# Kernel optimization log

Measured on AMD Instinct MI355X. Metric: run time of the kernel, lower is better.

The kernel has to match this reference:

```python
import jax, jax.numpy as jnp
import numpy as np

DEPTH = 2          # number of transformer blocks
DIM = 1280         # hidden_size
NHEADS = 16
HDIM = DIM // NHEADS  # 80
FF = 5120          # intermediate_size
S = 8192           # total ragged tokens
NSEG = 8           # number of image segments
EPS = 1e-6
GRID = 32          # per-image patch grid side (32*32*8 = 8192)


def _rotate_half(x):
    h = x.shape[-1] // 2
    return jnp.concatenate([-x[..., h:], x[..., :h]], axis=-1)


def _layernorm(x, g, b):
    mu = jnp.mean(x, axis=-1, keepdims=True)
    var = jnp.mean(jnp.square(x - mu), axis=-1, keepdims=True)
    return (x - mu) * jax.lax.rsqrt(var + EPS) * g + b


def setup_inputs() -> dict:
    key = jax.random.key(0)
    ks = jax.random.split(key, 16)
    std = 0.02
    hidden_states = jax.random.normal(ks[0], (S, DIM), jnp.float32)
    cu_seqlens = jnp.arange(NSEG + 1, dtype=jnp.int32) * (S // NSEG)
    # 2D rotary: per-axis freq table of size head_dim//4, concat row+col -> head_dim//2,
    # duplicated (cat(freqs, freqs)) -> head_dim, then cos/sin.
    rot_dim = HDIM // 2
    inv_freq = 1.0 / (10000.0 ** (jnp.arange(0, rot_dim, 2, dtype=jnp.float32) / rot_dim))  # [HDIM//4]
    tok = jnp.arange(S)
    rows = ((tok % (GRID * GRID)) // GRID).astype(jnp.float32)
    cols = (tok % GRID).astype(jnp.float32)
    freqs = jnp.concatenate([rows[:, None] * inv_freq[None, :], cols[:, None] * inv_freq[None, :]], axis=-1)  # [S, HDIM//2]
    emb = jnp.concatenate([freqs, freqs], axis=-1)  # [S, HDIM]
    cos = jnp.cos(emb)
    sin = jnp.sin(emb)
    def rnd(k, shape):
        return jax.random.normal(k, shape, jnp.float32) * std
    params = {
        'ln1_g': jnp.ones((DEPTH, DIM), jnp.float32), 'ln1_b': jnp.zeros((DEPTH, DIM), jnp.float32),
        'ln2_g': jnp.ones((DEPTH, DIM), jnp.float32), 'ln2_b': jnp.zeros((DEPTH, DIM), jnp.float32),
        'qkv_w': rnd(ks[1], (DEPTH, 3 * DIM, DIM)), 'qkv_b': jnp.zeros((DEPTH, 3 * DIM), jnp.float32),
        'proj_w': rnd(ks[2], (DEPTH, DIM, DIM)), 'proj_b': jnp.zeros((DEPTH, DIM), jnp.float32),
        'fc1_w': rnd(ks[3], (DEPTH, FF, DIM)), 'fc1_b': jnp.zeros((DEPTH, FF), jnp.float32),
        'fc2_w': rnd(ks[4], (DEPTH, DIM, FF)), 'fc2_b': jnp.zeros((DEPTH, DIM), jnp.float32),
    }
    return dict(hidden_states=hidden_states, cu_seqlens=cu_seqlens, cos=cos, sin=sin, **params)


def reference(hidden_states, cu_seqlens, cos, sin,
              ln1_g, ln1_b, ln2_g, ln2_b,
              qkv_w, qkv_b, proj_w, proj_b,
              fc1_w, fc1_b, fc2_w, fc2_b):
    seq = hidden_states.shape[0]
    # cu_seqlens is a static (int) input; derive the block-diagonal segmentation.
    seg = np.diff(np.asarray(jax.device_get(cu_seqlens)))
    L = int(seg[0])
    assert (seg == L).all(), 'reference assumes equal-length segments'
    n = len(seg)
    scale = HDIM ** -0.5
    c = cos[:, None, :]  # broadcast over heads, like cos.unsqueeze(1)
    s_ = sin[:, None, :]
    x = hidden_states
    for i in range(DEPTH):
        # --- attention ---
        h = _layernorm(x, ln1_g[i], ln1_b[i])
        qkv = (h @ qkv_w[i].T + qkv_b[i]).reshape(seq, 3, NHEADS, HDIM)
        q, k, v = qkv[:, 0], qkv[:, 1], qkv[:, 2]
        q = q * c + _rotate_half(q) * s_
        k = k * c + _rotate_half(k) * s_
        qs = q.reshape(n, L, NHEADS, HDIM)
        ks_ = k.reshape(n, L, NHEADS, HDIM)
        vs = v.reshape(n, L, NHEADS, HDIM)
        # block-diagonal (per-segment) attention, fp32 softmax
        attn = jnp.einsum('nlhd,nkhd->nhlk', qs, ks_) * scale
        p = jax.nn.softmax(attn, axis=-1)
        o = jnp.einsum('nhlk,nkhd->nlhd', p, vs).reshape(seq, DIM)
        x = x + (o @ proj_w[i].T + proj_b[i])
        # --- mlp (gelu tanh approx) ---
        h2 = _layernorm(x, ln2_g[i], ln2_b[i])
        x = x + (jax.nn.gelu(h2 @ fc1_w[i].T + fc1_b[i], approximate=True) @ fc2_w[i].T + fc2_b[i])
    return x
```

## Files before the change

### kernel.cpp

```cpp
#include <hip/hip_runtime.h>
#include <hip/hip_bf16.h>

typedef __attribute__((ext_vector_type(8))) short bf16x8;
typedef __attribute__((ext_vector_type(4))) float f32x4;
typedef __attribute__((ext_vector_type(8))) unsigned short u16x8;

__device__ __forceinline__ void gload_lds16(const void* g, void* l) {
  __builtin_amdgcn_global_load_lds(
      (const __attribute__((address_space(1))) unsigned int*)g,
      (__attribute__((address_space(3))) unsigned int*)l, 16, 0, 0);
}

__device__ __forceinline__ unsigned short f2bfu(float f) {
  __hip_bfloat16 h = __float2bfloat16(f);
  return __builtin_bit_cast(unsigned short, h);
}

__global__ __launch_bounds__(256) void copy_f32(const float* __restrict__ in,
                                                float* __restrict__ out, int n) {
  for (int i = blockIdx.x * 256 + threadIdx.x; i < n; i += gridDim.x * 256)
    out[i] = in[i];
}

__global__ __launch_bounds__(256) void w2bf(const float* __restrict__ in,
                                            __hip_bfloat16* __restrict__ out, int n) {
  for (int i = blockIdx.x * 256 + threadIdx.x; i < n; i += gridDim.x * 256)
    out[i] = __float2bfloat16(in[i]);
}

__global__ __launch_bounds__(256) void ln_kernel(const float* __restrict__ x,
                                                 const float* __restrict__ g,
                                                 const float* __restrict__ b,
                                                 __hip_bfloat16* __restrict__ h) {
  const int row = blockIdx.x;
  const int tid = threadIdx.x;
  const float* xr = x + (size_t)row * 1280;
  float v[5];
  float s = 0.f;
#pragma unroll
  for (int i = 0; i < 5; i++) { v[i] = xr[tid + i * 256]; s += v[i]; }
#pragma unroll
  for (int off = 32; off >= 1; off >>= 1) s += __shfl_xor(s, off);
  __shared__ float red[8];
  const int w = tid >> 6, lane = tid & 63;
  if (lane == 0) red[w] = s;
  __syncthreads();
  const float mu = (red[0] + red[1] + red[2] + red[3]) * (1.f / 1280.f);
  float q = 0.f;
#pragma unroll
  for (int i = 0; i < 5; i++) { float d = v[i] - mu; q += d * d; }
#pragma unroll
  for (int off = 32; off >= 1; off >>= 1) q += __shfl_xor(q, off);
  if (lane == 0) red[4 + w] = q;
  __syncthreads();
  const float var = (red[4] + red[5] + red[6] + red[7]) * (1.f / 1280.f);
  const float rstd = rsqrtf(var + 1e-6f);
#pragma unroll
  for (int i = 0; i < 5; i++) {
    int c = tid + i * 256;
    h[(size_t)row * 1280 + c] = __float2bfloat16((v[i] - mu) * rstd * g[c] + b[c]);
  }
}

__global__ __launch_bounds__(256) void rope_kernel(__hip_bfloat16* __restrict__ qkv,
                                                   const float* __restrict__ cs,
                                                   const float* __restrict__ sn) {
  const int TOT = 8192 * 2 * 16 * 40;
  for (int idx = blockIdx.x * 256 + threadIdx.x; idx < TOT; idx += gridDim.x * 256) {
    int d = idx % 40;
    int t = idx / 40;
    int head = t & 15;
    int t2 = t >> 4;
    int part = t2 & 1;
    int s = t2 >> 1;
    size_t base = ((size_t)s * 3 + part) * 1280 + head * 80;
    float e0 = __bfloat162float(qkv[base + d]);
    float e1 = __bfloat162float(qkv[base + d + 40]);
    float c0 = cs[s * 80 + d];
    float s0 = sn[s * 80 + d];
    float c1 = cs[s * 80 + d + 40];
    float s1 = sn[s * 80 + d + 40];
    qkv[base + d]      = __float2bfloat16(e0 * c0 - e1 * s0);
    qkv[base + d + 40] = __float2bfloat16(e1 * c1 + e0 * s1);
  }
}

__global__ __launch_bounds__(256) void vtrans_kernel(const __hip_bfloat16* __restrict__ qkv,
                                                     __hip_bfloat16* __restrict__ vt) {
  const int idx = blockIdx.x * 256 + threadIdx.x;
  const int s = idx & 8191;
  const int dc = idx >> 13;
  const unsigned short* src = (const unsigned short*)qkv + ((size_t)s * 3 + 2) * 1280 + dc * 8;
  u16x8 v = *(const u16x8*)src;
  unsigned short* dst = (unsigned short*)vt + (size_t)dc * 8 * 8192 + s;
#pragma unroll
  for (int j = 0; j < 8; j++) dst[(size_t)j * 8192] = v[j];
}

#define VMCNT4 asm volatile("s_waitcnt vmcnt(4)" ::: "memory")

#define GPHASE(MH, NH, DOA, STG, VM)                                                       \
  do {                                                                                     \
    if (DOA) {                                                                             \
      _Pragma("unroll") for (int mm = 0; mm < 4; mm++)                                     \
      _Pragma("unroll") for (int kk = 0; kk < 2; kk++)                                     \
        af[mm][kk] = *(const bf16x8*)(lds + bufOff + (MH) * 16384 + rowA + mm * 2048 + sw_s[kk]); \
    }                                                                                      \
    bf16x8 bfr[2][2];                                                                      \
    _Pragma("unroll") for (int nn = 0; nn < 2; nn++)                                       \
    _Pragma("unroll") for (int kk = 0; kk < 2; kk++)                                       \
      bfr[nn][kk] = *(const bf16x8*)(lds + bufOff + (NH) * 16384 + rowB + nn * 2048 + sw_s[kk]); \
    STG;                                                                                   \
    __builtin_amdgcn_s_barrier();                                                          \
    __builtin_amdgcn_s_setprio(1);                                                         \
    _Pragma("unroll") for (int kk = 0; kk < 2; kk++)                                       \
    _Pragma("unroll") for (int mm = 0; mm < 4; mm++)                                       \
    _Pragma("unroll") for (int nn = 0; nn < 2; nn++)                                       \
      acc[(MH) * 4 + mm][(NH) * 2 + nn] = __builtin_amdgcn_mfma_f32_16x16x32_bf16(         \
          af[mm][kk], bfr[nn][kk], acc[(MH) * 4 + mm][(NH) * 2 + nn], 0, 0, 0);            \
    __builtin_amdgcn_s_setprio(0);                                                         \
    VM;                                                                                    \
    __builtin_amdgcn_s_barrier();                                                          \
  } while (0)

template <int EPI>
__global__ __launch_bounds__(512, 2) void gemm256(const __hip_bfloat16* __restrict__ A,
                                                  const __hip_bfloat16* __restrict__ B,
                                                  const float* __restrict__ bias,
                                                  __hip_bfloat16* __restrict__ C,
                                                  float* __restrict__ X,
                                                  int M, int N, int K) {
  __shared__ __align__(16) char lds[131072];
  const int tid = threadIdx.x, lane = tid & 63, w = tid >> 6;
  const int wr = w >> 2, wc = w & 3;
  const int lm = lane & 15, hi = lane >> 4;

  const int nby = M >> 8, nbx = N >> 8;
  const int nwg = nbx * nby;
  const int cpx = nwg >> 3;
  const int swg = (blockIdx.x & 7) * cpx + (blockIdx.x >> 3);
  const int by = swg % nby, bx = swg / nby;
  const long mBase = (long)by << 8, nBase = (long)bx << 8;

  f32x4 acc[8][4];
#pragma unroll
  for (int m = 0; m < 8; m++)
#pragma unroll
    for (int n = 0; n < 4; n++) acc[m][n] = (f32x4){0.f, 0.f, 0.f, 0.f};

  const int r0 = (w << 3) + (lane >> 3);
  const int slotT = (lane & 7) ^ (lane >> 3);
  const unsigned short* Ag = (const unsigned short*)A;
  const unsigned short* Bg = (const unsigned short*)B;
  const size_t aB = (size_t)(mBase + r0) * K + slotT * 8;
  const size_t bB = (size_t)(nBase + r0) * K + slotT * 8;
  const int wdst = w << 10;

  auto STAGE = [&](int tile, int half, int isB) {
    char* dst = lds + ((tile & 1) << 16) + (isB << 15) + (half << 14) + wdst;
    const unsigned short* src =
        (isB ? Bg + bB : Ag + aB) + (size_t)(half << 7) * (size_t)K + ((size_t)tile << 6);
    gload_lds16(src, dst);
    gload_lds16(src + ((size_t)K << 6), dst + 8192);
  };

  const int rowA = (wr * 64 + lm) * 128;
  const int rowB = (wc * 32 + lm) * 128 + 32768;
  const int key = lm & 7;
  int sw_s[2];
#pragma unroll
  for (int kk = 0; kk < 2; kk++) sw_s[kk] = (((kk << 2) | hi) ^ key) << 4;

  const int nt = K >> 6;

  STAGE(0, 0, 0); STAGE(0, 0, 1); STAGE(0, 1, 1); STAGE(0, 1, 0);
  STAGE(1, 0, 0); STAGE(1, 0, 1);
  VMCNT4;
  __builtin_amdgcn_s_barrier();

  for (int t = 0; t < nt; ++t) {
    const int bufOff = (t & 1) << 16;
    const bool s1 = t + 1 < nt, s2 = t + 2 < nt;
    bf16x8 af[4][2];
    GPHASE(0, 0, 1, if (s1) STAGE(t + 1, 1, 1), (void)0);
    GPHASE(0, 1, 0, if (s1) STAGE(t + 1, 1, 0), (void)0);
    GPHASE(1, 0, 1, if (s2) STAGE(t + 2, 0, 0), (void)0);
    GPHASE(1, 1, 0, if (s2) STAGE(t + 2, 0, 1), VMCNT4);
  }

#pragma unroll
  for (int n = 0; n < 4; n++) {
    const int col = (int)nBase + (n >> 1) * 128 + wc * 32 + (n & 1) * 16 + lm;
    const float bv = bias[col];
#pragma unroll
    for (int m = 0; m < 8; m++) {
      const int er = (int)mBase + (m >> 2) * 128 + wr * 64 + (m & 3) * 16 + hi * 4;
#pragma unroll
      for (int j = 0; j < 4; j++) {
        float v = acc[m][n][j] + bv;
        size_t off = (size_t)(er + j) * N + col;
        if constexpr (EPI == 0) {
          C[off] = __float2bfloat16(v);
        } else if constexpr (EPI == 1) {
          float u = v + 0.044715f * v * v * v;
          float E = exp2f(2.30220818f * u);
          float t = 1.f - 2.f / (E + 1.f);
          C[off] = __float2bfloat16(0.5f * v * (1.f + t));
        } else {
          X[off] += v;
        }
      }
    }
  }
}

__global__ __launch_bounds__(256) void attn_kernel(const __hip_bfloat16* __restrict__ qkv,
                                                   const __hip_bfloat16* __restrict__ vtg,
                                                   __hip_bfloat16* __restrict__ o) {
  __shared__ __align__(16) unsigned short Ks[64 * 96];
  __shared__ __align__(16) unsigned short Vt[80 * 72];
  __shared__ __align__(16) unsigned short Ps[4][16 * 72];
  const int tid = threadIdx.x, lane = tid & 63, w = tid >> 6;
  const int lm = lane & 15, hi = lane >> 4;
  const int qt = blockIdx.x, head = blockIdx.y, seg = blockIdx.z;
  const int s0 = seg * 1024;
  const int qrow0 = s0 + qt * 64;
  const unsigned short* qg = (const unsigned short*)qkv;
  const unsigned short* vg = (const unsigned short*)vtg + (size_t)head * 80 * 8192;

  for (int idx = tid; idx < 1024; idx += 256) {
    int r = idx >> 4, c = 80 + (idx & 15);
    Ks[r * 96 + c] = 0;
  }

  bf16x8 aq[3];
  {
    const unsigned short* qrow = qg + (size_t)(qrow0 + w * 16 + lm) * 3840 + head * 80;
#pragma unroll
    for (int kk = 0; kk < 3; kk++) aq[kk] = *(const bf16x8*)(qrow + kk * 32 + hi * 8);
  }

  float m_s[4] = {-1e30f, -1e30f, -1e30f, -1e30f};
  float l_s[4] = {0.f, 0.f, 0.f, 0.f};
  f32x4 accO[5];
#pragma unroll
  for (int nf = 0; nf < 5; nf++) accO[nf] = (f32x4){0.f, 0.f, 0.f, 0.f};

  const float SM = 0.11180339887498949f * 1.4426950408889634f;

  for (int kt = 0; kt < 16; kt++) {
    __syncthreads();
    for (int c = tid; c < 640; c += 256) {
      int r = c / 10, c8 = c % 10;
      *(u16x8*)&Ks[r * 96 + c8 * 8] =
          *(const u16x8*)(qg + ((size_t)(s0 + kt * 64 + r) * 3 + 1) * 1280 + head * 80 + c8 * 8);
    }
    for (int c = tid; c < 640; c += 256) {
      int d = c >> 3, sc = c & 7;
      *(u16x8*)&Vt[d * 72 + sc * 8] =
          *(const u16x8*)(vg + (size_t)d * 8192 + s0 + kt * 64 + sc * 8);
    }
    __syncthreads();

    f32x4 sf[4];
#pragma unroll
    for (int n = 0; n < 4; n++) sf[n] = (f32x4){0.f, 0.f, 0.f, 0.f};
#pragma unroll
    for (int kk = 0; kk < 3; kk++) {
#pragma unroll
      for (int n = 0; n < 4; n++) {
        bf16x8 bk = *(const bf16x8*)(&Ks[(n * 16 + lm) * 96 + kk * 32 + hi * 8]);
        sf[n] = __builtin_amdgcn_mfma_f32_16x16x32_bf16(aq[kk], bk, sf[n], 0, 0, 0);
      }
    }

    float alpha[4];
#pragma unroll
    for (int j = 0; j < 4; j++) {
      float v = fmaxf(fmaxf(sf[0][j], sf[1][j]), fmaxf(sf[2][j], sf[3][j]));
#pragma unroll
      for (int off = 1; off < 16; off <<= 1) v = fmaxf(v, __shfl_xor(v, off));
      float mn = fmaxf(m_s[j], v);
      alpha[j] = exp2f((m_s[j] - mn) * SM);
      m_s[j] = mn;
    }
    float rsum[4] = {0.f, 0.f, 0.f, 0.f};
#pragma unroll
    for (int n = 0; n < 4; n++)
#pragma unroll
      for (int j = 0; j < 4; j++) {
        float p = exp2f((sf[n][j] - m_s[j]) * SM);
        sf[n][j] = p;
        rsum[j] += p;
      }
#pragma unroll
    for (int j = 0; j < 4; j++) {
#pragma unroll
      for (int off = 1; off < 16; off <<= 1) rsum[j] += __shfl_xor(rsum[j], off);
      l_s[j] = l_s[j] * alpha[j] + rsum[j];
    }
#pragma unroll
    for (int nf = 0; nf < 5; nf++)
#pragma unroll
      for (int j = 0; j < 4; j++) accO[nf][j] *= alpha[j];

#pragma unroll
    for (int n = 0; n < 4; n++)
#pragma unroll
      for (int j = 0; j < 4; j++)
        Ps[w][(hi * 4 + j) * 72 + n * 16 + lm] = f2bfu(sf[n][j]);

#pragma unroll
    for (int kk = 0; kk < 2; kk++) {
      bf16x8 pa = *(const bf16x8*)(&Ps[w][lm * 72 + kk * 32 + hi * 8]);
#pragma unroll
      for (int nf = 0; nf < 5; nf++) {
        bf16x8 bv = *(const bf16x8*)(&Vt[(nf * 16 + lm) * 72 + kk * 32 + hi * 8]);
        accO[nf] = __builtin_amdgcn_mfma_f32_16x16x32_bf16(pa, bv, accO[nf], 0, 0, 0);
      }
    }
  }

#pragma unroll
  for (int nf = 0; nf < 5; nf++) {
    int d = nf * 16 + lm;
#pragma unroll
    for (int j = 0; j < 4; j++) {
      int r = qrow0 + w * 16 + hi * 4 + j;
      o[(size_t)r * 1280 + head * 80 + d] = __float2bfloat16(accO[nf][j] / l_s[j]);
    }
  }
}

extern "C" void kernel_launch(void* const* d_in, const int* in_sizes, int n_in,
                              void* d_out, int out_size, void* d_ws, size_t ws_size,
                              hipStream_t stream) {
  (void)in_sizes; (void)n_in; (void)out_size; (void)ws_size;
  const float* hidden = (const float*)d_in[0];
  const float* cs   = (const float*)d_in[2];
  const float* sn   = (const float*)d_in[3];
  const float* ln1g = (const float*)d_in[4];
  const float* ln1b = (const float*)d_in[5];
  const float* ln2g = (const float*)d_in[6];
  const float* ln2b = (const float*)d_in[7];
  const float* qkvw = (const float*)d_in[8];
  const float* qkvb = (const float*)d_in[9];
  const float* pw   = (const float*)d_in[10];
  const float* pb   = (const float*)d_in[11];
  const float* f1w  = (const float*)d_in[12];
  const float* f1b  = (const float*)d_in[13];
  const float* f2w  = (const float*)d_in[14];
  const float* f2b  = (const float*)d_in[15];

  float* x = (float*)d_out;

  char* ws = (char*)d_ws;
  __hip_bfloat16* h    = (__hip_bfloat16*)ws;
  __hip_bfloat16* vt   = (__hip_bfloat16*)ws;
  __hip_bfloat16* qkv  = (__hip_bfloat16*)(ws + 20971520);
  __hip_bfloat16* o    = (__hip_bfloat16*)(ws + 83886080);
  __hip_bfloat16* ffh  = (__hip_bfloat16*)(ws + 20971520);
  __hip_bfloat16* wbuf = (__hip_bfloat16*)(ws + 104857600);

  const int NTOK = 8192 * 1280;
  copy_f32<<<2048, 256, 0, stream>>>(hidden, x, NTOK);
  for (int i = 0; i < 2; i++) {
    ln_kernel<<<8192, 256, 0, stream>>>(x, ln1g + i * 1280, ln1b + i * 1280, h);

    w2bf<<<2048, 256, 0, stream>>>(qkvw + (size_t)i * 3840 * 1280, wbuf, 3840 * 1280);
    gemm256<0><<<480, 512, 0, stream>>>(h, wbuf, qkvb + i * 3840, qkv, nullptr,
                                        8192, 3840, 1280);
    vtrans_kernel<<<5120, 256, 0, stream>>>(qkv, vt);
    rope_kernel<<<4096, 256, 0, stream>>>(qkv, cs, sn);
    attn_kernel<<<dim3(16, 16, 8), 256, 0, stream>>>(qkv, vt, o);

    w2bf<<<2048, 256, 0, stream>>>(pw + (size_t)i * 1280 * 1280, wbuf, 1280 * 1280);
    gemm256<2><<<160, 512, 0, stream>>>(o, wbuf, pb + i * 1280, nullptr, x,
                                        8192, 1280, 1280);

    ln_kernel<<<8192, 256, 0, stream>>>(x, ln2g + i * 1280, ln2b + i * 1280, h);

    w2bf<<<2048, 256, 0, stream>>>(f1w + (size_t)i * 5120 * 1280, wbuf, 5120 * 1280);
    gemm256<1><<<640, 512, 0, stream>>>(h, wbuf, f1b + i * 5120, ffh, nullptr,
                                        8192, 5120, 1280);

    w2bf<<<2048, 256, 0, stream>>>(f2w + (size_t)i * 1280 * 5120, wbuf, 1280 * 5120);
    gemm256<2><<<160, 512, 0, stream>>>(ffh, wbuf, f2b + i * 1280, nullptr, x,
                                        8192, 1280, 5120);
  }
}
```

Baseline: 1.442 ms.

## Load K and V fragments directly from global memory in attention, doubling KV tile

The attention kernel stops staging K and V tiles in shared memory and instead has each wave read its MFMA B-operand fragments straight from global memory, which removes both block-wide barriers per tile. The KV tile grows from 64 to 128 keys, so there are half as many online-softmax rescale steps. The zero padding of the head dimension from 80 to 96 moves from the K tile in shared memory onto the Q fragment in registers. The cost is that the four waves in a block now each re-read the same K/V data through the caches with strided, less coalesced accesses, and register pressure rises from holding eight score fragments.

```diff
diff --git a/kernel.cpp b/kernel.cpp
--- a/kernel.cpp
+++ b/kernel.cpp
@@ -217,8 +217,6 @@
 __global__ __launch_bounds__(256) void attn_kernel(const __hip_bfloat16* __restrict__ qkv,
                                                    const __hip_bfloat16* __restrict__ vtg,
                                                    __hip_bfloat16* __restrict__ o) {
-  __shared__ __align__(16) unsigned short Ks[64 * 96];
-  __shared__ __align__(16) unsigned short Vt[80 * 72];
   __shared__ __align__(16) unsigned short Ps[4][16 * 72];
   const int tid = threadIdx.x, lane = tid & 63, w = tid >> 6;
   const int lm = lane & 15, hi = lane >> 4;
@@ -226,18 +224,15 @@
   const int s0 = seg * 1024;
   const int qrow0 = s0 + qt * 64;
   const unsigned short* qg = (const unsigned short*)qkv;
+  const unsigned short* kg = qg + 1280 + head * 80;
   const unsigned short* vg = (const unsigned short*)vtg + (size_t)head * 80 * 8192;
-
-  for (int idx = tid; idx < 1024; idx += 256) {
-    int r = idx >> 4, c = 80 + (idx & 15);
-    Ks[r * 96 + c] = 0;
-  }
 
   bf16x8 aq[3];
   {
     const unsigned short* qrow = qg + (size_t)(qrow0 + w * 16 + lm) * 3840 + head * 80;
 #pragma unroll
     for (int kk = 0; kk < 3; kk++) aq[kk] = *(const bf16x8*)(qrow + kk * 32 + hi * 8);
+    if (hi >= 2) aq[2] = (bf16x8){0, 0, 0, 0, 0, 0, 0, 0};
   }
 
   float m_s[4] = {-1e30f, -1e30f, -1e30f, -1e30f};
@@ -248,28 +243,18 @@
 
   const float SM = 0.11180339887498949f * 1.4426950408889634f;
 
-  for (int kt = 0; kt < 16; kt++) {
-    __syncthreads();
-    for (int c = tid; c < 640; c += 256) {
-      int r = c / 10, c8 = c % 10;
-      *(u16x8*)&Ks[r * 96 + c8 * 8] =
-          *(const u16x8*)(qg + ((size_t)(s0 + kt * 64 + r) * 3 + 1) * 1280 + head * 80 + c8 * 8);
-    }
-    for (int c = tid; c < 640; c += 256) {
-      int d = c >> 3, sc = c & 7;
-      *(u16x8*)&Vt[d * 72 + sc * 8] =
-          *(const u16x8*)(vg + (size_t)d * 8192 + s0 + kt * 64 + sc * 8);
-    }
-    __syncthreads();
-
-    f32x4 sf[4];
-#pragma unroll
-    for (int n = 0; n < 4; n++) sf[n] = (f32x4){0.f, 0.f, 0.f, 0.f};
-#pragma unroll
-    for (int kk = 0; kk < 3; kk++) {
-#pragma unroll
-      for (int n = 0; n < 4; n++) {
-        bf16x8 bk = *(const bf16x8*)(&Ks[(n * 16 + lm) * 96 + kk * 32 + hi * 8]);
+  for (int kt = 0; kt < 8; kt++) {
+    const int kv0 = s0 + kt * 128;
+
+    f32x4 sf[8];
+#pragma unroll
+    for (int n = 0; n < 8; n++) sf[n] = (f32x4){0.f, 0.f, 0.f, 0.f};
+#pragma unroll
+    for (int n = 0; n < 8; n++) {
+      const unsigned short* krow = kg + (size_t)(kv0 + n * 16 + lm) * 3840;
+#pragma unroll
+      for (int kk = 0; kk < 3; kk++) {
+        bf16x8 bk = *(const bf16x8*)(krow + kk * 32 + hi * 8);
         sf[n] = __builtin_amdgcn_mfma_f32_16x16x32_bf16(aq[kk], bk, sf[n], 0, 0, 0);
       }
     }
@@ -277,7 +262,9 @@
     float alpha[4];
 #pragma unroll
     for (int j = 0; j < 4; j++) {
-      float v = fmaxf(fmaxf(sf[0][j], sf[1][j]), fmaxf(sf[2][j], sf[3][j]));
+      float v = sf[0][j];
+#pragma unroll
+      for (int n = 1; n < 8; n++) v = fmaxf(v, sf[n][j]);
 #pragma unroll
       for (int off = 1; off < 16; off <<= 1) v = fmaxf(v, __shfl_xor(v, off));
       float mn = fmaxf(m_s[j], v);
@@ -286,7 +273,7 @@
     }
     float rsum[4] = {0.f, 0.f, 0.f, 0.f};
 #pragma unroll
-    for (int n = 0; n < 4; n++)
+    for (int n = 0; n < 8; n++)
 #pragma unroll
       for (int j = 0; j < 4; j++) {
         float p = exp2f((sf[n][j] - m_s[j]) * SM);
@@ -305,18 +292,21 @@
       for (int j = 0; j < 4; j++) accO[nf][j] *= alpha[j];
 
 #pragma unroll
-    for (int n = 0; n < 4; n++)
-#pragma unroll
-      for (int j = 0; j < 4; j++)
-        Ps[w][(hi * 4 + j) * 72 + n * 16 + lm] = f2bfu(sf[n][j]);
-
-#pragma unroll
-    for (int kk = 0; kk < 2; kk++) {
-      bf16x8 pa = *(const bf16x8*)(&Ps[w][lm * 72 + kk * 32 + hi * 8]);
-#pragma unroll
-      for (int nf = 0; nf < 5; nf++) {
-        bf16x8 bv = *(const bf16x8*)(&Vt[(nf * 16 + lm) * 72 + kk * 32 + hi * 8]);
-        accO[nf] = __builtin_amdgcn_mfma_f32_16x16x32_bf16(pa, bv, accO[nf], 0, 0, 0);
+    for (int h = 0; h < 2; h++) {
+#pragma unroll
+      for (int n = 0; n < 4; n++)
+#pragma unroll
+        for (int j = 0; j < 4; j++)
+          Ps[w][(hi * 4 + j) * 72 + n * 16 + lm] = f2bfu(sf[h * 4 + n][j]);
+#pragma unroll
+      for (int kk = 0; kk < 2; kk++) {
+        bf16x8 pa = *(const bf16x8*)(&Ps[w][lm * 72 + kk * 32 + hi * 8]);
+#pragma unroll
+        for (int nf = 0; nf < 5; nf++) {
+          bf16x8 bv = *(const bf16x8*)(vg + (size_t)(nf * 16 + lm) * 8192 +
+                                       kv0 + h * 64 + kk * 32 + hi * 8);
+          accO[nf] = __builtin_amdgcn_mfma_f32_16x16x32_bf16(pa, bv, accO[nf], 0, 0, 0);
+        }
       }
     }
   }
```

After: 1.875 ms. +30.0%, slower.

## Prefetch next K/V tile into registers in attention and repad P buffer

Applied to the files above, without the earlier changes.

The attention loop now loads the next K and V tile from global memory into registers before computing on the current tile. Those registers are written to shared memory after the current tile's MFMA work, with barriers around the write. This is meant to hide global load latency behind the QK^T, softmax and PV computation. The per-wave P staging buffer row stride also changes from 72 to 68 elements to alter the LDS bank mapping. The 68-element stride makes 16-byte vector reads of P misaligned, and the prefetch raises register pressure.

```diff
diff --git a/kernel.cpp b/kernel.cpp
--- a/kernel.cpp
+++ b/kernel.cpp
@@ -219,7 +219,7 @@
                                                    __hip_bfloat16* __restrict__ o) {
   __shared__ __align__(16) unsigned short Ks[64 * 96];
   __shared__ __align__(16) unsigned short Vt[80 * 72];
-  __shared__ __align__(16) unsigned short Ps[4][16 * 72];
+  __shared__ __align__(16) unsigned short Ps[4][16 * 68];
   const int tid = threadIdx.x, lane = tid & 63, w = tid >> 6;
   const int lm = lane & 15, hi = lane >> 4;
   const int qt = blockIdx.x, head = blockIdx.y, seg = blockIdx.z;
@@ -240,6 +240,39 @@
     for (int kk = 0; kk < 3; kk++) aq[kk] = *(const bf16x8*)(qrow + kk * 32 + hi * 8);
   }
 
+  auto loadKV = [&](int kt, u16x8* kr, u16x8* vr) {
+#pragma unroll
+    for (int it = 0; it < 3; it++) {
+      int c = tid + it * 256;
+      if (c < 640) {
+        int r = c / 10, c8 = c % 10;
+        kr[it] = *(const u16x8*)(qg + ((size_t)(s0 + kt * 64 + r) * 3 + 1) * 1280 +
+                                 head * 80 + c8 * 8);
+        int d = c >> 3, sc = c & 7;
+        vr[it] = *(const u16x8*)(vg + (size_t)d * 8192 + s0 + kt * 64 + sc * 8);
+      }
+    }
+  };
+  auto writeKV = [&](u16x8* kr, u16x8* vr) {
+#pragma unroll
+    for (int it = 0; it < 3; it++) {
+      int c = tid + it * 256;
+      if (c < 640) {
+        int r = c / 10, c8 = c % 10;
+        *(u16x8*)&Ks[r * 96 + c8 * 8] = kr[it];
+        int d = c >> 3, sc = c & 7;
+        *(u16x8*)&Vt[d * 72 + sc * 8] = vr[it];
+      }
+    }
+  };
+
+  {
+    u16x8 kr[3], vr[3];
+    loadKV(0, kr, vr);
+    writeKV(kr, vr);
+  }
+  __syncthreads();
+
   float m_s[4] = {-1e30f, -1e30f, -1e30f, -1e30f};
   float l_s[4] = {0.f, 0.f, 0.f, 0.f};
   f32x4 accO[5];
@@ -249,18 +282,8 @@
   const float SM = 0.11180339887498949f * 1.4426950408889634f;
 
   for (int kt = 0; kt < 16; kt++) {
-    __syncthreads();
-    for (int c = tid; c < 640; c += 256) {
-      int r = c / 10, c8 = c % 10;
-      *(u16x8*)&Ks[r * 96 + c8 * 8] =
-          *(const u16x8*)(qg + ((size_t)(s0 + kt * 64 + r) * 3 + 1) * 1280 + head * 80 + c8 * 8);
-    }
-    for (int c = tid; c < 640; c += 256) {
-      int d = c >> 3, sc = c & 7;
-      *(u16x8*)&Vt[d * 72 + sc * 8] =
-          *(const u16x8*)(vg + (size_t)d * 8192 + s0 + kt * 64 + sc * 8);
-    }
-    __syncthreads();
+    u16x8 krn[3], vrn[3];
+    if (kt + 1 < 16) loadKV(kt + 1, krn, vrn);
 
     f32x4 sf[4];
 #pragma unroll
@@ -308,17 +331,21 @@
     for (int n = 0; n < 4; n++)
 #pragma unroll
       for (int j = 0; j < 4; j++)
-        Ps[w][(hi * 4 + j) * 72 + n * 16 + lm] = f2bfu(sf[n][j]);
+        Ps[w][(hi * 4 + j) * 68 + n * 16 + lm] = f2bfu(sf[n][j]);
 
 #pragma unroll
     for (int kk = 0; kk < 2; kk++) {
-      bf16x8 pa = *(const bf16x8*)(&Ps[w][lm * 72 + kk * 32 + hi * 8]);
+      bf16x8 pa = *(const bf16x8*)(&Ps[w][lm * 68 + kk * 32 + hi * 8]);
 #pragma unroll
       for (int nf = 0; nf < 5; nf++) {
         bf16x8 bv = *(const bf16x8*)(&Vt[(nf * 16 + lm) * 72 + kk * 32 + hi * 8]);
         accO[nf] = __builtin_amdgcn_mfma_f32_16x16x32_bf16(pa, bv, accO[nf], 0, 0, 0);
       }
     }
+
+    __syncthreads();
+    if (kt + 1 < 16) writeKV(krn, vrn);
+    __syncthreads();
   }
 
 #pragma unroll
```

Result: faster. 1.413 ms (-2.0%).
